# Kernel tuning notes

Measured on AMD Instinct MI355X. Metric: run time of the kernel, lower is better.

Reference implementation:

```python
import jax, jax.numpy as jnp
import numpy as np

B, N, D_IN, D_OUT = 8, 2048, 1024, 1024


def setup_inputs() -> dict:
    key = jax.random.key(0)
    k0, k1, k2, k3 = jax.random.split(key, 4)
    scale = 1.0 / np.sqrt(D_IN)
    x = jax.random.normal(k0, (B, N, D_IN), dtype=jnp.float32)
    Wq = jax.random.normal(k1, (D_IN, D_OUT), dtype=jnp.float32) * scale
    Wk = jax.random.normal(k2, (D_IN, D_OUT), dtype=jnp.float32) * scale
    Wv = jax.random.normal(k3, (D_IN, D_OUT), dtype=jnp.float32) * scale
    return {"x": x, "Wq": Wq, "Wk": Wk, "Wv": Wv}


def reference(x, Wq, Wk, Wv):
    # x: [b, n, d_in]; single-head causal attention, dropout p=0 (eval).
    q = jnp.einsum('bnd,de->bne', x, Wq)
    k = jnp.einsum('bnd,de->bne', x, Wk)
    v = jnp.einsum('bnd,de->bne', x, Wv)
    n = x.shape[1]
    scores = jnp.einsum('bqe,bke->bqk', q, k)  # [b, n, n]
    causal_mask = jnp.triu(jnp.ones((n, n), dtype=bool), k=1)
    scores = jnp.where(causal_mask, -jnp.inf, scores)
    scale = 1.0 / jnp.sqrt(jnp.asarray(k.shape[-1], dtype=scores.dtype))
    attn = jax.nn.softmax(scores * scale, axis=-1)
    context = jnp.einsum('bqk,bke->bqe', attn, v)
    return context
```

## Files before the change

kernel.cpp:

```cpp
#include <hip/hip_runtime.h>


typedef unsigned short u16;
typedef __bf16 bf16x8 __attribute__((ext_vector_type(8)));
typedef float f32x4 __attribute__((ext_vector_type(4)));
typedef unsigned short u16x8 __attribute__((ext_vector_type(8)));
typedef unsigned short u16x4 __attribute__((ext_vector_type(4)));

static constexpr int BATCH = 8;
static constexpr int SEQ = 2048;
static constexpr int DIM = 1024;

static constexpr size_t SZ_XB = (size_t)BATCH * SEQ * DIM * 2;
static constexpr size_t SZ_W  = (size_t)DIM * DIM * 2;
static constexpr size_t OFF_XB  = 0;
static constexpr size_t OFF_WQT = OFF_XB + SZ_XB;
static constexpr size_t OFF_WKT = OFF_WQT + SZ_W;
static constexpr size_t OFF_WVT = OFF_WKT + SZ_W;
static constexpr size_t OFF_Q   = OFF_WVT + SZ_W;
static constexpr size_t OFF_K   = OFF_Q + SZ_XB;
static constexpr size_t OFF_VT  = OFF_K + SZ_XB;
static constexpr size_t OFF_E   = OFF_VT + SZ_XB;

__device__ __forceinline__ u16 f2b(float f) {
  unsigned u = __builtin_bit_cast(unsigned, f);
  u += 0x7fffu + ((u >> 16) & 1u);
  return (u16)(u >> 16);
}

__device__ __forceinline__ void gload16(const u16* g, u16* l) {
  __builtin_amdgcn_global_load_lds((__attribute__((address_space(1))) void*)g,
                                   (__attribute__((address_space(3))) void*)l, 16, 0, 0);
}

#define VWAIT(N) asm volatile("s_waitcnt vmcnt(" #N ")" ::: "memory")

__device__ __forceinline__ void barrier_raw() {
  __builtin_amdgcn_sched_barrier(0);
  __builtin_amdgcn_s_barrier();
  __builtin_amdgcn_sched_barrier(0);
}

__global__ __launch_bounds__(256) void cast_f32_bf16(const float* __restrict__ in,
                                                     u16* __restrict__ out) {
  const size_t i = ((size_t)blockIdx.x * 256 + threadIdx.x) * 8;
  float4 a = *(const float4*)(in + i);
  float4 b = *(const float4*)(in + i + 4);
  u16x8 o;
  o[0] = f2b(a.x); o[1] = f2b(a.y); o[2] = f2b(a.z); o[3] = f2b(a.w);
  o[4] = f2b(b.x); o[5] = f2b(b.y); o[6] = f2b(b.z); o[7] = f2b(b.w);
  *reinterpret_cast<u16x8*>(out + i) = o;
}

__global__ __launch_bounds__(256) void transpose_cast_w(const float* __restrict__ W,
                                                        u16* __restrict__ WT) {
  __shared__ float t[32][33];
  const int k0 = blockIdx.x * 32, n0 = blockIdx.y * 32;
  const int tx = threadIdx.x, ty = threadIdx.y;
#pragma unroll
  for (int dy = 0; dy < 32; dy += 8)
    t[ty + dy][tx] = W[(size_t)(k0 + ty + dy) * DIM + n0 + tx];
  __syncthreads();
#pragma unroll
  for (int dy = 0; dy < 32; dy += 8)
    WT[(size_t)(n0 + ty + dy) * DIM + k0 + tx] = f2b(t[tx][ty + dy]);
}

template <int MODE>
__global__ __launch_bounds__(512, 4) void gemm128(
    const u16* __restrict__ A, size_t sA, int lda,
    const u16* __restrict__ Bt, size_t sB, int ldb,
    void* __restrict__ C, size_t sC, int ldc,
    int Kdim, float scale) {
  const int bx = blockIdx.x, bz = blockIdx.z;
  const int by = (MODE == 3) ? (int)(gridDim.y - 1 - blockIdx.y) : (int)blockIdx.y;
  if (MODE == 2 && 2 * bx > by) return;
  const u16* Ab = A + (size_t)bz * sA;
  const u16* Bb = Bt + (size_t)bz * sB;
  const int rowTile = by * 128, colTile = bx * 256;
  int kmax = Kdim;
  if (MODE == 3) {
    int km = (by + 1) * 128;
    if (km < kmax) kmax = km;
  }
  const int NT = kmax >> 5;

  __shared__ __align__(16) u16 lds[3 * 12288];

  const int tid = threadIdx.x;
  const int w = tid >> 6, l = tid & 63;
  const int wm = w >> 2, wn = w & 3;
  const int lr = l & 15, quad = l >> 4;

  auto srow = [](int c) { int u = (c & 7) ^ ((c >> 3) & 7); return 2 * (c >> 3) + (u >> 2); };
  auto skq  = [](int c) { int u = (c & 7) ^ ((c >> 3) & 7); return u & 3; };
  const u16* pA0 = Ab + (size_t)(rowTile + srow(tid)) * lda + skq(tid) * 8;
  const u16* pB0 = Bb + (size_t)(colTile + srow(tid)) * ldb + skq(tid) * 8;
  const u16* pB1 = Bb + (size_t)(colTile + srow(tid + 512)) * ldb + skq(tid + 512) * 8;

  int offA[4], offB[4];
#pragma unroll
  for (int mi = 0; mi < 4; ++mi) {
    const int row = wm * 64 + mi * 16 + lr;
    offA[mi] = ((row * 64 + quad * 16) ^ (((row >> 1) & 7) << 4)) >> 1;
  }
#pragma unroll
  for (int ni = 0; ni < 4; ++ni) {
    const int row = wn * 64 + ni * 16 + lr;
    offB[ni] = 4096 + ((((row * 64 + quad * 16) ^ (((row >> 1) & 7) << 4))) >> 1);
  }

  f32x4 acc[4][4];
#pragma unroll
  for (int i = 0; i < 4; ++i)
#pragma unroll
    for (int j = 0; j < 4; ++j) acc[i][j] = (f32x4){0.f, 0.f, 0.f, 0.f};
  float rsum[4] = {0.f, 0.f, 0.f, 0.f};

#define STAGE(tt)                                   \
  {                                                 \
    u16* sb = &lds[((unsigned)(tt) % 3u) * 12288];  \
    const int ko = (tt) * 32;                       \
    gload16(pA0 + ko, sb + w * 512);                \
    gload16(pB0 + ko, sb + 4096 + w * 512);         \
    gload16(pB1 + ko, sb + 8192 + w * 512);         \
  }

  STAGE(0);
  STAGE(1);
  VWAIT(3);
  barrier_raw();

  for (int t = 0; t < NT; ++t) {
    const u16* S = &lds[((unsigned)t % 3u) * 12288];
    bf16x8 af[4], bf[4];
#pragma unroll
    for (int mi = 0; mi < 4; ++mi)
      af[mi] = *reinterpret_cast<const bf16x8*>(&S[offA[mi]]);
#pragma unroll
    for (int ni = 0; ni < 4; ++ni)
      bf[ni] = *reinterpret_cast<const bf16x8*>(&S[offB[ni]]);
    if (t + 2 < NT) STAGE(t + 2);
    if (MODE == 3) {
#pragma unroll
      for (int mi = 0; mi < 4; ++mi) {
        float s = 0.f;
#pragma unroll
        for (int j = 0; j < 8; ++j) s += (float)af[mi][j];
        rsum[mi] += s;
      }
    }
    __builtin_amdgcn_s_setprio(1);
#pragma unroll
    for (int mi = 0; mi < 4; ++mi)
#pragma unroll
      for (int ni = 0; ni < 4; ++ni)
        acc[mi][ni] =
            __builtin_amdgcn_mfma_f32_16x16x32_bf16(af[mi], bf[ni], acc[mi][ni], 0, 0, 0);
    __builtin_amdgcn_s_setprio(0);
    if (t + 2 < NT) {
      VWAIT(3);
    } else if (t + 1 < NT) {
      VWAIT(0);
    }
    asm volatile("s_waitcnt lgkmcnt(0)" ::: "memory");
    barrier_raw();
  }
#undef STAGE

  if (MODE == 3) {
#pragma unroll
    for (int mi = 0; mi < 4; ++mi) {
      rsum[mi] += __shfl_xor(rsum[mi], 16);
      rsum[mi] += __shfl_xor(rsum[mi], 32);
    }
  }

  const int orow0 = rowTile + wm * 64 + quad * 4;
  const int ocol0 = colTile + wn * 64 + lr;
#pragma unroll
  for (int mi = 0; mi < 4; ++mi) {
    float linv[4];
    if (MODE == 3) {
#pragma unroll
      for (int r = 0; r < 4; ++r) linv[r] = 1.f / __shfl(rsum[mi], quad * 4 + r);
    }
#pragma unroll
    for (int ni = 0; ni < 4; ++ni) {
      const int colg = ocol0 + ni * 16;
      if (MODE == 1) {
        const int rowg0 = orow0 + mi * 16;
        const int bb = rowg0 >> 11, nn = rowg0 & (SEQ - 1);
        u16x4 pk;
#pragma unroll
        for (int r = 0; r < 4; ++r) pk[r] = f2b(acc[mi][ni][r]);
        *reinterpret_cast<u16x4*>(&((u16*)C)[(size_t)bb * sC + (size_t)colg * ldc + nn]) = pk;
      } else {
#pragma unroll
        for (int r = 0; r < 4; ++r) {
          const int rowg = orow0 + mi * 16 + r;
          const float v = acc[mi][ni][r];
          if (MODE == 0) {
            ((u16*)C)[(size_t)bz * sC + (size_t)rowg * ldc + colg] = f2b(v);
          } else if (MODE == 2) {
            const float e = (colg <= rowg) ? __expf(v * scale) : 0.f;
            ((u16*)C)[(size_t)bz * sC + (size_t)rowg * ldc + colg] = f2b(e);
          } else {
            ((float*)C)[(size_t)bz * sC + (size_t)rowg * ldc + colg] = v * linv[r];
          }
        }
      }
    }
  }
}

extern "C" void kernel_launch(void* const* d_in, const int* in_sizes, int n_in,
                              void* d_out, int out_size, void* d_ws, size_t ws_size,
                              hipStream_t stream) {
  const float* x = (const float*)d_in[0];
  const float* Wq = (const float*)d_in[1];
  const float* Wk = (const float*)d_in[2];
  const float* Wv = (const float*)d_in[3];
  float* out = (float*)d_out;
  char* ws = (char*)d_ws;

  u16* xb = (u16*)(ws + OFF_XB);
  u16* wqT = (u16*)(ws + OFF_WQT);
  u16* wkT = (u16*)(ws + OFF_WKT);
  u16* wvT = (u16*)(ws + OFF_WVT);
  u16* qb = (u16*)(ws + OFF_Q);
  u16* kb = (u16*)(ws + OFF_K);
  u16* vt = (u16*)(ws + OFF_VT);
  u16* eb = (u16*)(ws + OFF_E);

  const int total = BATCH * SEQ * DIM;
  cast_f32_bf16<<<total / (256 * 8), 256, 0, stream>>>(x, xb);
  transpose_cast_w<<<dim3(32, 32), dim3(32, 8), 0, stream>>>(Wq, wqT);
  transpose_cast_w<<<dim3(32, 32), dim3(32, 8), 0, stream>>>(Wk, wkT);
  transpose_cast_w<<<dim3(32, 32), dim3(32, 8), 0, stream>>>(Wv, wvT);

  gemm128<0><<<dim3(4, 128, 1), 512, 0, stream>>>(xb, 0, DIM, wqT, 0, DIM, qb, 0, DIM,
                                                  DIM, 1.f);
  gemm128<0><<<dim3(4, 128, 1), 512, 0, stream>>>(xb, 0, DIM, wkT, 0, DIM, kb, 0, DIM,
                                                  DIM, 1.f);
  gemm128<1><<<dim3(4, 128, 1), 512, 0, stream>>>(xb, 0, DIM, wvT, 0, DIM, vt,
                                                  (size_t)DIM * SEQ, SEQ, DIM, 1.f);
  gemm128<2><<<dim3(8, 16, BATCH), 512, 0, stream>>>(
      qb, (size_t)SEQ * DIM, DIM, kb, (size_t)SEQ * DIM, DIM, eb, (size_t)SEQ * SEQ, SEQ,
      DIM, 0.03125f);
  gemm128<3><<<dim3(4, 16, BATCH), 512, 0, stream>>>(
      eb, (size_t)SEQ * SEQ, SEQ, vt, (size_t)DIM * SEQ, SEQ, out, (size_t)SEQ * DIM, DIM,
      SEQ, 1.f);
}
```

Before: 392.7 us.

## Fuse QKV projections into one GEMM and compute softmax row sums in score epilogue

The three Q/K/V projection GEMMs become a single launch over 12 column tiles. This relies on the transposed weights sitting next to each other in the workspace, and the epilogue routes each tile to the Q, K or transposed V buffer. Softmax denominators are no longer summed from A fragments inside the PV GEMM main loop. Instead the exp-score epilogue reduces the bf16-rounded values per row and atomically adds them into a zeroed workspace array. The PV tile order is also changed so half the batches run rows in forward order, which affects load balance. The atomics and the extra memset add some cost.

```diff
diff --git a/kernel.cpp b/kernel.cpp
--- a/kernel.cpp
+++ b/kernel.cpp
@@ -21,11 +21,16 @@
 static constexpr size_t OFF_K   = OFF_Q + SZ_XB;
 static constexpr size_t OFF_VT  = OFF_K + SZ_XB;
 static constexpr size_t OFF_E   = OFF_VT + SZ_XB;
+static constexpr size_t OFF_RS  = OFF_E + (size_t)BATCH * SEQ * SEQ * 2;
 
 __device__ __forceinline__ u16 f2b(float f) {
   unsigned u = __builtin_bit_cast(unsigned, f);
   u += 0x7fffu + ((u >> 16) & 1u);
   return (u16)(u >> 16);
+}
+
+__device__ __forceinline__ float b2f(u16 b) {
+  return __builtin_bit_cast(float, ((unsigned)b) << 16);
 }
 
 __device__ __forceinline__ void gload16(const u16* g, u16* l) {
@@ -71,9 +76,11 @@
     const u16* __restrict__ A, size_t sA, int lda,
     const u16* __restrict__ Bt, size_t sB, int ldb,
     void* __restrict__ C, size_t sC, int ldc,
-    int Kdim, float scale) {
+    int Kdim, float scale,
+    void* __restrict__ C2, void* __restrict__ C3, float* __restrict__ rs) {
   const int bx = blockIdx.x, bz = blockIdx.z;
-  const int by = (MODE == 3) ? (int)(gridDim.y - 1 - blockIdx.y) : (int)blockIdx.y;
+  int by = (int)blockIdx.y;
+  if (MODE == 3) by = (bz < 4) ? (15 - by) : by;
   if (MODE == 2 && 2 * bx > by) return;
   const u16* Ab = A + (size_t)bz * sA;
   const u16* Bb = Bt + (size_t)bz * sB;
@@ -115,7 +122,6 @@
   for (int i = 0; i < 4; ++i)
 #pragma unroll
     for (int j = 0; j < 4; ++j) acc[i][j] = (f32x4){0.f, 0.f, 0.f, 0.f};
-  float rsum[4] = {0.f, 0.f, 0.f, 0.f};
 
 #define STAGE(tt)                                   \
   {                                                 \
@@ -141,15 +147,6 @@
     for (int ni = 0; ni < 4; ++ni)
       bf[ni] = *reinterpret_cast<const bf16x8*>(&S[offB[ni]]);
     if (t + 2 < NT) STAGE(t + 2);
-    if (MODE == 3) {
-#pragma unroll
-      for (int mi = 0; mi < 4; ++mi) {
-        float s = 0.f;
-#pragma unroll
-        for (int j = 0; j < 8; ++j) s += (float)af[mi][j];
-        rsum[mi] += s;
-      }
-    }
     __builtin_amdgcn_s_setprio(1);
 #pragma unroll
     for (int mi = 0; mi < 4; ++mi)
@@ -168,46 +165,83 @@
   }
 #undef STAGE
 
-  if (MODE == 3) {
-#pragma unroll
-    for (int mi = 0; mi < 4; ++mi) {
-      rsum[mi] += __shfl_xor(rsum[mi], 16);
-      rsum[mi] += __shfl_xor(rsum[mi], 32);
-    }
-  }
-
   const int orow0 = rowTile + wm * 64 + quad * 4;
   const int ocol0 = colTile + wn * 64 + lr;
-#pragma unroll
-  for (int mi = 0; mi < 4; ++mi) {
-    float linv[4];
-    if (MODE == 3) {
-#pragma unroll
-      for (int r = 0; r < 4; ++r) linv[r] = 1.f / __shfl(rsum[mi], quad * 4 + r);
-    }
-#pragma unroll
-    for (int ni = 0; ni < 4; ++ni) {
-      const int colg = ocol0 + ni * 16;
-      if (MODE == 1) {
+
+  if (MODE == 4) {
+    const int which = colTile >> 10;
+    if (which < 2) {
+      u16* dst = (which == 0) ? (u16*)C : (u16*)C2;
+      const int colL0 = ocol0 & 1023;
+#pragma unroll
+      for (int mi = 0; mi < 4; ++mi)
+#pragma unroll
+        for (int ni = 0; ni < 4; ++ni) {
+          const int colg = colL0 + ni * 16;
+#pragma unroll
+          for (int r = 0; r < 4; ++r) {
+            const int rowg = orow0 + mi * 16 + r;
+            dst[(size_t)rowg * DIM + colg] = f2b(acc[mi][ni][r]);
+          }
+        }
+    } else {
+      u16* dst = (u16*)C3;
+      const int colL0 = ocol0 & 1023;
+#pragma unroll
+      for (int mi = 0; mi < 4; ++mi) {
         const int rowg0 = orow0 + mi * 16;
         const int bb = rowg0 >> 11, nn = rowg0 & (SEQ - 1);
-        u16x4 pk;
-#pragma unroll
-        for (int r = 0; r < 4; ++r) pk[r] = f2b(acc[mi][ni][r]);
-        *reinterpret_cast<u16x4*>(&((u16*)C)[(size_t)bb * sC + (size_t)colg * ldc + nn]) = pk;
-      } else {
+#pragma unroll
+        for (int ni = 0; ni < 4; ++ni) {
+          const int colg = colL0 + ni * 16;
+          u16x4 pk;
+#pragma unroll
+          for (int r = 0; r < 4; ++r) pk[r] = f2b(acc[mi][ni][r]);
+          *reinterpret_cast<u16x4*>(
+              &dst[(size_t)bb * ((size_t)DIM * SEQ) + (size_t)colg * SEQ + nn]) = pk;
+        }
+      }
+    }
+  } else if (MODE == 2) {
+#pragma unroll
+    for (int mi = 0; mi < 4; ++mi) {
+      float rloc[4] = {0.f, 0.f, 0.f, 0.f};
+#pragma unroll
+      for (int ni = 0; ni < 4; ++ni) {
+        const int colg = ocol0 + ni * 16;
 #pragma unroll
         for (int r = 0; r < 4; ++r) {
           const int rowg = orow0 + mi * 16 + r;
-          const float v = acc[mi][ni][r];
-          if (MODE == 0) {
-            ((u16*)C)[(size_t)bz * sC + (size_t)rowg * ldc + colg] = f2b(v);
-          } else if (MODE == 2) {
-            const float e = (colg <= rowg) ? __expf(v * scale) : 0.f;
-            ((u16*)C)[(size_t)bz * sC + (size_t)rowg * ldc + colg] = f2b(e);
-          } else {
-            ((float*)C)[(size_t)bz * sC + (size_t)rowg * ldc + colg] = v * linv[r];
-          }
+          const float e = (colg <= rowg) ? __expf(acc[mi][ni][r] * scale) : 0.f;
+          const u16 pk = f2b(e);
+          ((u16*)C)[(size_t)bz * sC + (size_t)rowg * ldc + colg] = pk;
+          rloc[r] += b2f(pk);
+        }
+      }
+#pragma unroll
+      for (int r = 0; r < 4; ++r) {
+        float v = rloc[r];
+        v += __shfl_xor(v, 1);
+        v += __shfl_xor(v, 2);
+        v += __shfl_xor(v, 4);
+        v += __shfl_xor(v, 8);
+        if (lr == 0) atomicAdd(&rs[bz * SEQ + orow0 + mi * 16 + r], v);
+      }
+    }
+  } else {
+#pragma unroll
+    for (int mi = 0; mi < 4; ++mi) {
+      float linv[4];
+#pragma unroll
+      for (int r = 0; r < 4; ++r) linv[r] = 1.f / rs[bz * SEQ + orow0 + mi * 16 + r];
+#pragma unroll
+      for (int ni = 0; ni < 4; ++ni) {
+        const int colg = ocol0 + ni * 16;
+#pragma unroll
+        for (int r = 0; r < 4; ++r) {
+          const int rowg = orow0 + mi * 16 + r;
+          ((float*)C)[(size_t)bz * sC + (size_t)rowg * ldc + colg] =
+              acc[mi][ni][r] * linv[r];
         }
       }
     }
@@ -232,23 +266,21 @@
   u16* kb = (u16*)(ws + OFF_K);
   u16* vt = (u16*)(ws + OFF_VT);
   u16* eb = (u16*)(ws + OFF_E);
+  float* rsum = (float*)(ws + OFF_RS);
 
   const int total = BATCH * SEQ * DIM;
   cast_f32_bf16<<<total / (256 * 8), 256, 0, stream>>>(x, xb);
   transpose_cast_w<<<dim3(32, 32), dim3(32, 8), 0, stream>>>(Wq, wqT);
   transpose_cast_w<<<dim3(32, 32), dim3(32, 8), 0, stream>>>(Wk, wkT);
   transpose_cast_w<<<dim3(32, 32), dim3(32, 8), 0, stream>>>(Wv, wvT);
-
-  gemm128<0><<<dim3(4, 128, 1), 512, 0, stream>>>(xb, 0, DIM, wqT, 0, DIM, qb, 0, DIM,
-                                                  DIM, 1.f);
-  gemm128<0><<<dim3(4, 128, 1), 512, 0, stream>>>(xb, 0, DIM, wkT, 0, DIM, kb, 0, DIM,
-                                                  DIM, 1.f);
-  gemm128<1><<<dim3(4, 128, 1), 512, 0, stream>>>(xb, 0, DIM, wvT, 0, DIM, vt,
-                                                  (size_t)DIM * SEQ, SEQ, DIM, 1.f);
+  hipMemsetAsync(rsum, 0, (size_t)BATCH * SEQ * sizeof(float), stream);
+
+  gemm128<4><<<dim3(12, 128, 1), 512, 0, stream>>>(
+      xb, 0, DIM, wqT, 0, DIM, qb, 0, DIM, DIM, 1.f, kb, vt, nullptr);
   gemm128<2><<<dim3(8, 16, BATCH), 512, 0, stream>>>(
       qb, (size_t)SEQ * DIM, DIM, kb, (size_t)SEQ * DIM, DIM, eb, (size_t)SEQ * SEQ, SEQ,
-      DIM, 0.03125f);
+      DIM, 0.03125f, nullptr, nullptr, rsum);
   gemm128<3><<<dim3(4, 16, BATCH), 512, 0, stream>>>(
       eb, (size_t)SEQ * SEQ, SEQ, vt, (size_t)DIM * SEQ, SEQ, out, (size_t)SEQ * DIM, DIM,
-      SEQ, 1.f);
-}
+      SEQ, 1.f, nullptr, nullptr, rsum);
+}
```

Result: faster. 365.4 us (-7.0%).
